# Kernel tuning notes

Measured on AMD Instinct MI355X. Metric: run time of the kernel, lower is better.

The kernel has to match this reference:

```python
import jax, jax.numpy as jnp
import numpy as np

B, S, E, H = 2, 2048, 1024, 16
D = E // H  # head dim = 64


def setup_inputs() -> dict:
    key = jax.random.key(0)
    k1, k2, k3 = jax.random.split(key, 3)
    x = jax.random.normal(k1, (B, S, E), dtype=jnp.float32)
    W_attn = jax.random.normal(k2, (E, 3 * E), dtype=jnp.float32) * (1.0 / np.sqrt(E))
    b_attn = jnp.zeros((3 * E,), dtype=jnp.float32)
    W_proj = jax.random.normal(k3, (E, E), dtype=jnp.float32) * (1.0 / np.sqrt(E))
    b_proj = jnp.zeros((E,), dtype=jnp.float32)
    return {"x": x, "W_attn": W_attn, "b_attn": b_attn, "W_proj": W_proj, "b_proj": b_proj}


def reference(x, W_attn, b_attn, W_proj, b_proj):
    b, s, e = x.shape
    qkv = x @ W_attn + b_attn                      # (B, S, 3E)
    q, k, v = jnp.split(qkv, 3, axis=-1)
    # (B, S, E) -> (B, H, S, D)
    def heads(t):
        return t.reshape(b, s, H, D).transpose(0, 2, 1, 3)
    q, k, v = heads(q), heads(k), heads(v)
    scale = 1.0 / np.sqrt(D)
    # ring QK^T over world_size=1 == full QK^T; scores (B, H, S, S)
    attn = jnp.einsum("bhqd,bhkd->bhqk", q, k) * scale
    causal = jnp.tril(jnp.ones((s, s), dtype=bool))
    attn = jnp.where(causal[None, None], attn, -jnp.inf)
    attn = jax.nn.softmax(attn, axis=-1)
    # ring AV over world_size=1 == full AV
    y = jnp.einsum("bhqk,bhkd->bhqd", attn, v)     # (B, H, S, D)
    y = y.transpose(0, 2, 1, 3).reshape(b, s, e)   # (B, S, E)
    return y @ W_proj + b_proj
```

## Files before the change

kernel.cpp:

```cpp
#include <hip/hip_runtime.h>
#include <hip/hip_bf16.h>

#define B_ 2
#define S_ 2048
#define E_ 1024
#define H_ 16
#define D_ 64

typedef __attribute__((ext_vector_type(8))) _Float16 half8;
typedef __attribute__((ext_vector_type(4))) _Float16 half4;
typedef __attribute__((ext_vector_type(4))) float floatx4;

__device__ inline void gload16(const _Float16* g, _Float16* l) {
    __builtin_amdgcn_global_load_lds(
        (const __attribute__((address_space(1))) void*)g,
        (__attribute__((address_space(3))) void*)l, 16, 0, 0);
}

__global__ __launch_bounds__(256) void k_prep(const float* __restrict__ x, _Float16* __restrict__ xh,
                                              const float* __restrict__ Wa, _Float16* __restrict__ Wat,
                                              const float* __restrict__ Wp, _Float16* __restrict__ Wpt) {
    __shared__ _Float16 tile[32][33];
    int bid = blockIdx.x, tid = threadIdx.x;
    if (bid < 2048) {
        int i = (bid * 256 + tid) * 8;
        float4 a = *(const float4*)(x + i);
        float4 b = *(const float4*)(x + i + 4);
        half8 o;
        o[0] = (_Float16)a.x; o[1] = (_Float16)a.y; o[2] = (_Float16)a.z; o[3] = (_Float16)a.w;
        o[4] = (_Float16)b.x; o[5] = (_Float16)b.y; o[6] = (_Float16)b.z; o[7] = (_Float16)b.w;
        *(half8*)(xh + i) = o;
        return;
    }
    const float* in;
    _Float16* out;
    int R, C, bx, by;
    if (bid < 5120) {
        int t = bid - 2048;
        in = Wa; out = Wat; R = E_; C = 3 * E_;
        bx = t % 96; by = t / 96;
    } else {
        int t = bid - 5120;
        in = Wp; out = Wpt; R = E_; C = E_;
        bx = t & 31; by = t >> 5;
    }
    int tx = tid & 31, ty = tid >> 5;
    int c0 = bx * 32, r0 = by * 32;
#pragma unroll
    for (int k = 0; k < 4; k++) {
        int r = ty + k * 8;
        tile[r][tx] = (_Float16)in[(size_t)(r0 + r) * C + c0 + tx];
    }
    __syncthreads();
#pragma unroll
    for (int k = 0; k < 4; k++) {
        int r = ty + k * 8;
        out[(size_t)(c0 + r) * R + r0 + tx] = tile[tx][r];
    }
}

template <int MODE>
__global__ __launch_bounds__(256) void k_gemm(const _Float16* __restrict__ A,
                                              const _Float16* __restrict__ Bt,
                                              const float* __restrict__ bias,
                                              void* __restrict__ out0,
                                              _Float16* __restrict__ out1,
                                              _Float16* __restrict__ out2,
                                              int M, int N, int K) {
    __shared__ __align__(16) _Float16 AsB[2 * 4096];
    __shared__ __align__(16) _Float16 BsB[2 * 4096];
    int tid = threadIdx.x;
    int lane = tid & 63, w = tid >> 6;
    int wm = w >> 1, wn = w & 1;
    int l15 = lane & 15, quad = lane >> 4;
    int nbx = N >> 7;
    int xcd = blockIdx.x & 7, s = blockIdx.x >> 3;
    int by = xcd * 4 + s / nbx;
    int bx = s % nbx;
    int m0 = by * 128, n0 = bx * 128;

    floatx4 acc[4][4];
    floatx4 zero = {0.f, 0.f, 0.f, 0.f};
#pragma unroll
    for (int i = 0; i < 4; i++)
#pragma unroll
        for (int j = 0; j < 4; j++) acc[i][j] = zero;

    int srow = tid >> 2;
    int scol = ((tid * 8) & 31) ^ ((srow & 3) << 3);
    const _Float16* aS0 = A + (size_t)(m0 + srow) * K + scol;
    const _Float16* aS1 = A + (size_t)(m0 + 64 + srow) * K + scol;
    const _Float16* bS0 = Bt + (size_t)(n0 + srow) * K + scol;
    const _Float16* bS1 = Bt + (size_t)(n0 + 64 + srow) * K + scol;

#define GSTAGE(ko_, buf_)                                          \
    do {                                                           \
        gload16(aS0 + (ko_), AsB + (buf_) * 4096 + w * 512);       \
        gload16(aS1 + (ko_), AsB + (buf_) * 4096 + 2048 + w * 512);\
        gload16(bS0 + (ko_), BsB + (buf_) * 4096 + w * 512);       \
        gload16(bS1 + (ko_), BsB + (buf_) * 4096 + 2048 + w * 512);\
    } while (0)

    GSTAGE(0, 0);
    int cur = 0;
    int sx = (l15 & 3) << 3;
    for (int k0 = 0; k0 < K; k0 += 32) {
        __syncthreads();
        if (k0 + 32 < K) GSTAGE(k0 + 32, cur ^ 1);
        const _Float16* AC = AsB + cur * 4096;
        const _Float16* BC = BsB + cur * 4096;
        half8 af[4], bfr[4];
#pragma unroll
        for (int i = 0; i < 4; i++)
            af[i] = *(const half8*)&AC[(wm * 64 + i * 16 + l15) * 32 + ((quad * 8) ^ sx)];
#pragma unroll
        for (int j = 0; j < 4; j++)
            bfr[j] = *(const half8*)&BC[(wn * 64 + j * 16 + l15) * 32 + ((quad * 8) ^ sx)];
#pragma unroll
        for (int i = 0; i < 4; i++)
#pragma unroll
            for (int j = 0; j < 4; j++)
                acc[i][j] = __builtin_amdgcn_mfma_f32_16x16x32_f16(af[i], bfr[j], acc[i][j], 0, 0, 0);
        cur ^= 1;
    }
#undef GSTAGE

    __syncthreads();
    _Float16* Ew = (w < 2 ? AsB : BsB) + (w & 1) * 4096;
    int gr0 = m0 + wm * 64;
    int gc0 = n0 + wn * 64;
    float bj[4];
#pragma unroll
    for (int j = 0; j < 4; j++) bj[j] = bias[gc0 + j * 16 + l15];

    if (MODE == 1) {
        float* Ef = (float*)Ew;
        float* outf = (float*)out0;
#pragma unroll
        for (int ip = 0; ip < 2; ip++) {
#pragma unroll
            for (int ii = 0; ii < 2; ii++) {
                int i = ip * 2 + ii;
#pragma unroll
                for (int j = 0; j < 4; j++)
#pragma unroll
                    for (int r = 0; r < 4; r++) {
                        int rl = ii * 16 + quad * 4 + r;
                        Ef[rl * 64 + ((j * 16 + l15) ^ ((rl & 7) << 2))] = acc[i][j][r] + bj[j];
                    }
            }
#pragma unroll
            for (int g = 0; g < 8; g++) {
                int rl = g * 4 + (lane >> 4);
                int c4 = (lane & 15) * 4;
                float4 v = *(float4*)&Ef[rl * 64 + (c4 ^ ((rl & 7) << 2))];
                *(float4*)&outf[(size_t)(gr0 + ip * 32 + rl) * N + gc0 + c4] = v;
            }
        }
    } else {
        int sect = gc0 >> 10;
        int hh = (gc0 & 1023) >> 6;
        int bb = gr0 >> 11, ss0 = gr0 & 2047;
        size_t hb = (size_t)(bb * H_ + hh);
        if (sect < 2) {
#pragma unroll
            for (int i = 0; i < 4; i++)
#pragma unroll
                for (int j = 0; j < 4; j++)
#pragma unroll
                    for (int r = 0; r < 4; r++) {
                        int rl = i * 16 + quad * 4 + r;
                        Ew[rl * 64 + ((j * 16 + l15) ^ ((rl & 7) << 3))] =
                            (_Float16)(acc[i][j][r] + bj[j]);
                    }
            _Float16* dst = (sect == 0 ? (_Float16*)out0 : out1) + (hb * S_ + ss0) * D_;
#pragma unroll
            for (int g = 0; g < 8; g++) {
                int rl = g * 8 + (lane >> 3);
                int c8 = (lane & 7) * 8;
                half8 v = *(const half8*)&Ew[rl * 64 + (c8 ^ ((rl & 7) << 3))];
                *(half8*)(dst + (size_t)rl * D_ + c8) = v;
            }
        } else {
#pragma unroll
            for (int i = 0; i < 4; i++)
#pragma unroll
                for (int j = 0; j < 4; j++) {
                    int dd = j * 16 + l15;
                    half4 pk;
#pragma unroll
                    for (int r = 0; r < 4; r++) pk[r] = (_Float16)(acc[i][j][r] + bj[j]);
                    *(half4*)&Ew[dd * 64 + ((i * 16 + quad * 4) ^ ((dd & 7) << 3))] = pk;
                }
#pragma unroll
            for (int g = 0; g < 8; g++) {
                int dd = g * 8 + (lane >> 3);
                int s8 = (lane & 7) * 8;
                half8 v = *(const half8*)&Ew[dd * 64 + (s8 ^ ((dd & 7) << 3))];
                *(half8*)(out2 + (hb * D_ + dd) * S_ + ss0 + s8) = v;
            }
        }
    }
}

__global__ __launch_bounds__(512, 4)
void k_attn(const _Float16* __restrict__ Qh,
            const _Float16* __restrict__ Kh,
            const _Float16* __restrict__ Vt,
            _Float16* __restrict__ y) {
    __shared__ __align__(16) _Float16 smem_h[25600];
    int tid = threadIdx.x;
    int lane = tid & 63, w = tid >> 6;
    int l15 = lane & 15, quad = lane >> 4;
    _Float16* KsB = smem_h;
    _Float16* VsB = smem_h + 8192;
    _Float16* Pw = smem_h + 16384 + w * (16 * 72);

    int bidx = blockIdx.x;
    int bh = 4 * (bidx & 7) + ((bidx >> 3) & 3);
    int qidx = (bidx >> 5) & 7;
    int qb = (bidx >> 8) ? qidx : (15 - qidx);
    int b = bh >> 4, h = bh & 15;

    const size_t hbase = (size_t)bh * (S_ * D_);
    const _Float16* Qp = Qh + hbase;
    const _Float16* Kp = Kh + hbase;
    const _Float16* Vp = Vt + hbase;

    int q0w = qb * 128 + 16 * w;
    int ktd = q0w >> 6;
    int ktmax = 2 * qb + 1;

    int r0 = tid >> 3;
    int cbh = ((tid * 8) & 63) ^ ((r0 & 7) << 3);
    const _Float16* kS = Kp + (size_t)r0 * D_ + cbh;
    const _Float16* vS = Vp + (size_t)r0 * S_ + cbh;

#define STAGE(kt_, buf_)                                             \
    do {                                                             \
        gload16(kS + (size_t)(kt_) * 4096, KsB + (buf_) * 4096 + w * 512); \
        gload16(vS + (size_t)(kt_) * 64, VsB + (buf_) * 4096 + w * 512);   \
    } while (0)

    half8 aq[2];
#pragma unroll
    for (int kk = 0; kk < 2; kk++) {
        half8 q = *(const half8*)(Qp + (size_t)(q0w + l15) * D_ + kk * 32 + quad * 8);
#pragma unroll
        for (int u = 0; u < 8; u++) q[u] *= (_Float16)0.125f;
        aq[kk] = q;
    }

    floatx4 zero = {0.f, 0.f, 0.f, 0.f};
    floatx4 o[4];
#pragma unroll
    for (int f = 0; f < 4; f++) o[f] = zero;
    float l_run = 0.f;

    STAGE(0, 0);
    int cur = 0;
    int swz = (l15 & 7) << 3;
    for (int kt = 0; kt <= ktmax; kt++) {
        __syncthreads();
        if (kt < ktmax) STAGE(kt + 1, cur ^ 1);
        if (kt <= ktd) {
            const _Float16* KC = KsB + cur * 4096;
            const _Float16* VC = VsB + cur * 4096;
            floatx4 sa[4];
#pragma unroll
            for (int jj = 0; jj < 4; jj++) {
                int row = jj * 16 + l15;
                half8 k0 = *(const half8*)&KC[row * 64 + ((quad * 8) ^ swz)];
                half8 k1 = *(const half8*)&KC[row * 64 + ((32 + quad * 8) ^ swz)];
                floatx4 a = zero;
                a = __builtin_amdgcn_mfma_f32_16x16x32_f16(k0, aq[0], a, 0, 0, 0);
                a = __builtin_amdgcn_mfma_f32_16x16x32_f16(k1, aq[1], a, 0, 0, 0);
                sa[jj] = a;
            }
            bool diag = (kt == ktd);
            int k64 = kt * 64;
            float ssum = 0.f;
#pragma unroll
            for (int jj = 0; jj < 4; jj++) {
                half4 pk;
#pragma unroll
                for (int r = 0; r < 4; r++) {
                    float v = __expf(sa[jj][r]);
                    if (diag) {
                        int key = k64 + jj * 16 + quad * 4 + r;
                        int query = q0w + l15;
                        if (key > query) v = 0.f;
                    }
                    ssum += v;
                    pk[r] = (_Float16)v;
                }
                *(half4*)&Pw[l15 * 72 + jj * 16 + quad * 4] = pk;
            }
            ssum += __shfl_xor(ssum, 16);
            ssum += __shfl_xor(ssum, 32);
            l_run += ssum;
#pragma unroll
            for (int kk = 0; kk < 2; kk++) {
                half8 ap = *(const half8*)&Pw[l15 * 72 + kk * 32 + quad * 8];
#pragma unroll
                for (int f = 0; f < 4; f++) {
                    int row = f * 16 + l15;
                    half8 bv = *(const half8*)&VC[row * 64 + ((kk * 32 + quad * 8) ^ swz)];
                    o[f] = __builtin_amdgcn_mfma_f32_16x16x32_f16(ap, bv, o[f], 0, 0, 0);
                }
            }
        }
        cur ^= 1;
    }
#undef STAGE

    float linv[4];
#pragma unroll
    for (int r = 0; r < 4; r++) linv[r] = 1.0f / __shfl(l_run, quad * 4 + r);
#pragma unroll
    for (int f = 0; f < 4; f++)
#pragma unroll
        for (int r = 0; r < 4; r++) {
            int row = q0w + quad * 4 + r;
            y[((size_t)(b * S_ + row)) * E_ + h * D_ + f * 16 + l15] =
                (_Float16)(o[f][r] * linv[r]);
        }
}

extern "C" void kernel_launch(void* const* d_in, const int* in_sizes, int n_in,
                              void* d_out, int out_size, void* d_ws, size_t ws_size,
                              hipStream_t stream) {
    const float* x      = (const float*)d_in[0];
    const float* W_attn = (const float*)d_in[1];
    const float* b_attn = (const float*)d_in[2];
    const float* W_proj = (const float*)d_in[3];
    const float* b_proj = (const float*)d_in[4];
    float* out = (float*)d_out;

    const int M = B_ * S_;
    char* ws = (char*)d_ws;
    _Float16* xh  = (_Float16*)ws; ws += (size_t)M * E_ * 2;
    _Float16* Wat = (_Float16*)ws; ws += (size_t)3 * E_ * E_ * 2;
    _Float16* Wpt = (_Float16*)ws; ws += (size_t)E_ * E_ * 2;
    _Float16* Qh  = (_Float16*)ws; ws += (size_t)M * E_ * 2;
    _Float16* Kh  = (_Float16*)ws; ws += (size_t)M * E_ * 2;
    _Float16* Vt  = (_Float16*)ws; ws += (size_t)M * E_ * 2;
    _Float16* yh  = xh;

    k_prep<<<6144, 256, 0, stream>>>(x, xh, W_attn, Wat, W_proj, Wpt);
    k_gemm<0><<<768, 256, 0, stream>>>(xh, Wat, b_attn, Qh, Kh, Vt, M, 3 * E_, E_);
    k_attn<<<512, 512, 0, stream>>>(Qh, Kh, Vt, yh);
    k_gemm<1><<<256, 256, 0, stream>>>(yh, Wpt, b_proj, (void*)out, nullptr, nullptr, M, E_, E_);
}
```

Baseline: 180.9 us.

## Shrink attention blocks to 64 queries and load V directly from global

The attention kernel now uses 256-thread blocks covering 64 query rows each, with twice as many blocks, so there are no idle warps on non-diagonal tiles and causal load balance is finer. V is no longer staged through LDS. Each warp reads its V fragments straight from global memory into registers, which halves LDS use and frees room for more resident blocks. The risk is higher global and L2 traffic for V, since each warp re-reads the same tile, and more K tile reloads across the smaller blocks.

```diff
diff --git a/kernel.cpp b/kernel.cpp
--- a/kernel.cpp
+++ b/kernel.cpp
@@ -203,23 +203,22 @@
     }
 }
 
-__global__ __launch_bounds__(512, 4)
+__global__ __launch_bounds__(256) __attribute__((amdgpu_waves_per_eu(2, 4)))
 void k_attn(const _Float16* __restrict__ Qh,
             const _Float16* __restrict__ Kh,
             const _Float16* __restrict__ Vt,
             _Float16* __restrict__ y) {
-    __shared__ __align__(16) _Float16 smem_h[25600];
+    __shared__ __align__(16) _Float16 smem_h[12800];
     int tid = threadIdx.x;
     int lane = tid & 63, w = tid >> 6;
     int l15 = lane & 15, quad = lane >> 4;
     _Float16* KsB = smem_h;
-    _Float16* VsB = smem_h + 8192;
-    _Float16* Pw = smem_h + 16384 + w * (16 * 72);
+    _Float16* Pw = smem_h + 8192 + w * (16 * 72);
 
     int bidx = blockIdx.x;
     int bh = 4 * (bidx & 7) + ((bidx >> 3) & 3);
-    int qidx = (bidx >> 5) & 7;
-    int qb = (bidx >> 8) ? qidx : (15 - qidx);
+    int qi = (bidx >> 5) & 15;
+    int qb = (bidx >> 9) ? (2 * qi) : (31 - 2 * qi);
     int b = bh >> 4, h = bh & 15;
 
     const size_t hbase = (size_t)bh * (S_ * D_);
@@ -227,19 +226,18 @@
     const _Float16* Kp = Kh + hbase;
     const _Float16* Vp = Vt + hbase;
 
-    int q0w = qb * 128 + 16 * w;
-    int ktd = q0w >> 6;
-    int ktmax = 2 * qb + 1;
+    int q0w = qb * 64 + 16 * w;
+    int ktmax = qb;
 
     int r0 = tid >> 3;
     int cbh = ((tid * 8) & 63) ^ ((r0 & 7) << 3);
-    const _Float16* kS = Kp + (size_t)r0 * D_ + cbh;
-    const _Float16* vS = Vp + (size_t)r0 * S_ + cbh;
-
-#define STAGE(kt_, buf_)                                             \
-    do {                                                             \
-        gload16(kS + (size_t)(kt_) * 4096, KsB + (buf_) * 4096 + w * 512); \
-        gload16(vS + (size_t)(kt_) * 64, VsB + (buf_) * 4096 + w * 512);   \
+    const _Float16* kS0 = Kp + (size_t)r0 * D_ + cbh;
+    const _Float16* kS1 = Kp + (size_t)(r0 + 32) * D_ + cbh;
+
+#define STAGE(kt_, buf_)                                                      \
+    do {                                                                      \
+        gload16(kS0 + (size_t)(kt_) * 4096, KsB + (buf_) * 4096 + w * 512);   \
+        gload16(kS1 + (size_t)(kt_) * 4096, KsB + (buf_) * 4096 + 2048 + w * 512); \
     } while (0)
 
     half8 aq[2];
@@ -261,54 +259,54 @@
     int cur = 0;
     int swz = (l15 & 7) << 3;
     for (int kt = 0; kt <= ktmax; kt++) {
+        int k64 = kt * 64;
         __syncthreads();
         if (kt < ktmax) STAGE(kt + 1, cur ^ 1);
-        if (kt <= ktd) {
-            const _Float16* KC = KsB + cur * 4096;
-            const _Float16* VC = VsB + cur * 4096;
-            floatx4 sa[4];
-#pragma unroll
-            for (int jj = 0; jj < 4; jj++) {
-                int row = jj * 16 + l15;
-                half8 k0 = *(const half8*)&KC[row * 64 + ((quad * 8) ^ swz)];
-                half8 k1 = *(const half8*)&KC[row * 64 + ((32 + quad * 8) ^ swz)];
-                floatx4 a = zero;
-                a = __builtin_amdgcn_mfma_f32_16x16x32_f16(k0, aq[0], a, 0, 0, 0);
-                a = __builtin_amdgcn_mfma_f32_16x16x32_f16(k1, aq[1], a, 0, 0, 0);
-                sa[jj] = a;
-            }
-            bool diag = (kt == ktd);
-            int k64 = kt * 64;
-            float ssum = 0.f;
-#pragma unroll
-            for (int jj = 0; jj < 4; jj++) {
-                half4 pk;
-#pragma unroll
-                for (int r = 0; r < 4; r++) {
-                    float v = __expf(sa[jj][r]);
-                    if (diag) {
-                        int key = k64 + jj * 16 + quad * 4 + r;
-                        int query = q0w + l15;
-                        if (key > query) v = 0.f;
-                    }
-                    ssum += v;
-                    pk[r] = (_Float16)v;
+        half8 bv[4][2];
+#pragma unroll
+        for (int f = 0; f < 4; f++)
+#pragma unroll
+            for (int kk = 0; kk < 2; kk++)
+                bv[f][kk] = *(const half8*)(Vp + (size_t)(f * 16 + l15) * S_ + k64 + kk * 32 + quad * 8);
+        const _Float16* KC = KsB + cur * 4096;
+        floatx4 sa[4];
+#pragma unroll
+        for (int jj = 0; jj < 4; jj++) {
+            int row = jj * 16 + l15;
+            half8 k0 = *(const half8*)&KC[row * 64 + ((quad * 8) ^ swz)];
+            half8 k1 = *(const half8*)&KC[row * 64 + ((32 + quad * 8) ^ swz)];
+            floatx4 a = zero;
+            a = __builtin_amdgcn_mfma_f32_16x16x32_f16(k0, aq[0], a, 0, 0, 0);
+            a = __builtin_amdgcn_mfma_f32_16x16x32_f16(k1, aq[1], a, 0, 0, 0);
+            sa[jj] = a;
+        }
+        bool diag = (kt == ktmax);
+        float ssum = 0.f;
+#pragma unroll
+        for (int jj = 0; jj < 4; jj++) {
+            half4 pk;
+#pragma unroll
+            for (int r = 0; r < 4; r++) {
+                float v = __expf(sa[jj][r]);
+                if (diag) {
+                    int key = k64 + jj * 16 + quad * 4 + r;
+                    int query = q0w + l15;
+                    if (key > query) v = 0.f;
                 }
-                *(half4*)&Pw[l15 * 72 + jj * 16 + quad * 4] = pk;
-            }
-            ssum += __shfl_xor(ssum, 16);
-            ssum += __shfl_xor(ssum, 32);
-            l_run += ssum;
-#pragma unroll
-            for (int kk = 0; kk < 2; kk++) {
-                half8 ap = *(const half8*)&Pw[l15 * 72 + kk * 32 + quad * 8];
-#pragma unroll
-                for (int f = 0; f < 4; f++) {
-                    int row = f * 16 + l15;
-                    half8 bv = *(const half8*)&VC[row * 64 + ((kk * 32 + quad * 8) ^ swz)];
-                    o[f] = __builtin_amdgcn_mfma_f32_16x16x32_f16(ap, bv, o[f], 0, 0, 0);
-                }
-            }
+                ssum += v;
+                pk[r] = (_Float16)v;
+            }
+            *(half4*)&Pw[l15 * 72 + jj * 16 + quad * 4] = pk;
+        }
+        ssum += __shfl_xor(ssum, 16);
+        ssum += __shfl_xor(ssum, 32);
+        l_run += ssum;
+#pragma unroll
+        for (int kk = 0; kk < 2; kk++) {
+            half8 ap = *(const half8*)&Pw[l15 * 72 + kk * 32 + quad * 8];
+#pragma unroll
+            for (int f = 0; f < 4; f++)
+                o[f] = __builtin_amdgcn_mfma_f32_16x16x32_f16(ap, bv[f][kk], o[f], 0, 0, 0);
         }
         cur ^= 1;
     }
@@ -349,6 +347,6 @@
 
     k_prep<<<6144, 256, 0, stream>>>(x, xh, W_attn, Wat, W_proj, Wpt);
     k_gemm<0><<<768, 256, 0, stream>>>(xh, Wat, b_attn, Qh, Kh, Vt, M, 3 * E_, E_);
-    k_attn<<<512, 512, 0, stream>>>(Qh, Kh, Vt, yh);
+    k_attn<<<1024, 256, 0, stream>>>(Qh, Kh, Vt, yh);
     k_gemm<1><<<256, 256, 0, stream>>>(yh, Wpt, b_proj, (void*)out, nullptr, nullptr, M, E_, E_);
 }
```

Result: slower. 211.0 us (+16.7%).

## Stage 128-key tiles per barrier with swizzled P buffer and MFMA priority hints

Applied to the files above, without the earlier changes.

Doubles the K/V tile staged per iteration from 64 to 128 keys, so there are half as many loop iterations and __syncthreads barriers. Each stage is processed as two 64-key sub-tiles, and warps whose queries fall below the second half of the diagonal tile skip it. The padded P scratch layout is replaced with an XOR-swizzled 64-wide layout, and s_setprio is raised around the MFMA sections. LDS use grows from about 50KB to 80KB per block, which may lower the number of resident blocks per CU.

```diff
diff --git a/kernel.cpp b/kernel.cpp
--- a/kernel.cpp
+++ b/kernel.cpp
@@ -208,13 +208,13 @@
             const _Float16* __restrict__ Kh,
             const _Float16* __restrict__ Vt,
             _Float16* __restrict__ y) {
-    __shared__ __align__(16) _Float16 smem_h[25600];
+    __shared__ __align__(16) _Float16 smem_h[40960];
     int tid = threadIdx.x;
     int lane = tid & 63, w = tid >> 6;
     int l15 = lane & 15, quad = lane >> 4;
     _Float16* KsB = smem_h;
-    _Float16* VsB = smem_h + 8192;
-    _Float16* Pw = smem_h + 16384 + w * (16 * 72);
+    _Float16* VsB = smem_h + 16384;
+    _Float16* Pw = smem_h + 32768 + w * 1024;
 
     int bidx = blockIdx.x;
     int bh = 4 * (bidx & 7) + ((bidx >> 3) & 3);
@@ -228,18 +228,20 @@
     const _Float16* Vp = Vt + hbase;
 
     int q0w = qb * 128 + 16 * w;
-    int ktd = q0w >> 6;
-    int ktmax = 2 * qb + 1;
 
     int r0 = tid >> 3;
     int cbh = ((tid * 8) & 63) ^ ((r0 & 7) << 3);
-    const _Float16* kS = Kp + (size_t)r0 * D_ + cbh;
-    const _Float16* vS = Vp + (size_t)r0 * S_ + cbh;
-
-#define STAGE(kt_, buf_)                                             \
-    do {                                                             \
-        gload16(kS + (size_t)(kt_) * 4096, KsB + (buf_) * 4096 + w * 512); \
-        gload16(vS + (size_t)(kt_) * 64, VsB + (buf_) * 4096 + w * 512);   \
+    const _Float16* kS0 = Kp + (size_t)r0 * D_ + cbh;
+    const _Float16* kS1 = Kp + (size_t)(r0 + 64) * D_ + cbh;
+    const _Float16* vS0 = Vp + (size_t)r0 * S_ + cbh;
+    const _Float16* vS1 = vS0 + 64;
+
+#define STAGE(kt_, buf_)                                                          \
+    do {                                                                          \
+        gload16(kS0 + (size_t)(kt_) * 8192, KsB + (buf_) * 8192 + w * 512);       \
+        gload16(kS1 + (size_t)(kt_) * 8192, KsB + (buf_) * 8192 + 4096 + w * 512);\
+        gload16(vS0 + (size_t)(kt_) * 128, VsB + (buf_) * 8192 + w * 512);        \
+        gload16(vS1 + (size_t)(kt_) * 128, VsB + (buf_) * 8192 + 4096 + w * 512); \
     } while (0)
 
     half8 aq[2];
@@ -260,13 +262,18 @@
     STAGE(0, 0);
     int cur = 0;
     int swz = (l15 & 7) << 3;
-    for (int kt = 0; kt <= ktmax; kt++) {
+    for (int kt = 0; kt <= qb; kt++) {
         __syncthreads();
-        if (kt < ktmax) STAGE(kt + 1, cur ^ 1);
-        if (kt <= ktd) {
-            const _Float16* KC = KsB + cur * 4096;
-            const _Float16* VC = VsB + cur * 4096;
+        if (kt < qb) STAGE(kt + 1, cur ^ 1);
+        bool diag = (kt == qb);
+#pragma unroll
+        for (int t = 0; t < 2; t++) {
+            if (diag && t == 1 && w < 4) break;
+            int k64 = kt * 128 + t * 64;
+            const _Float16* KC = KsB + cur * 8192 + t * 4096;
+            const _Float16* VC = VsB + cur * 8192 + t * 4096;
             floatx4 sa[4];
+            __builtin_amdgcn_s_setprio(1);
 #pragma unroll
             for (int jj = 0; jj < 4; jj++) {
                 int row = jj * 16 + l15;
@@ -277,8 +284,7 @@
                 a = __builtin_amdgcn_mfma_f32_16x16x32_f16(k1, aq[1], a, 0, 0, 0);
                 sa[jj] = a;
             }
-            bool diag = (kt == ktd);
-            int k64 = kt * 64;
+            __builtin_amdgcn_s_setprio(0);
             float ssum = 0.f;
 #pragma unroll
             for (int jj = 0; jj < 4; jj++) {
@@ -294,14 +300,15 @@
                     ssum += v;
                     pk[r] = (_Float16)v;
                 }
-                *(half4*)&Pw[l15 * 72 + jj * 16 + quad * 4] = pk;
+                *(half4*)&Pw[l15 * 64 + ((jj * 16 + quad * 4) ^ swz)] = pk;
             }
             ssum += __shfl_xor(ssum, 16);
             ssum += __shfl_xor(ssum, 32);
             l_run += ssum;
+            __builtin_amdgcn_s_setprio(1);
 #pragma unroll
             for (int kk = 0; kk < 2; kk++) {
-                half8 ap = *(const half8*)&Pw[l15 * 72 + kk * 32 + quad * 8];
+                half8 ap = *(const half8*)&Pw[l15 * 64 + ((kk * 32 + quad * 8) ^ swz)];
 #pragma unroll
                 for (int f = 0; f < 4; f++) {
                     int row = f * 16 + l15;
@@ -309,6 +316,7 @@
                     o[f] = __builtin_amdgcn_mfma_f32_16x16x32_f16(ap, bv, o[f], 0, 0, 0);
                 }
             }
+            __builtin_amdgcn_s_setprio(0);
         }
         cur ^= 1;
     }
```

After: 171.0 us. -5.4%, faster.
